# Performance work log

Measured on AMD Instinct MI355X. Metric: run time of the kernel, lower is better.

The kernel has to match this reference:

```python
import jax, jax.numpy as jnp
import numpy as np

K = 3
STRIDE = 1
PAD = 1
DIL = 1


def setup_inputs() -> dict:
    key = jax.random.key(0)
    k1, k2, k3 = jax.random.split(key, 3)
    B, C, O, H, W = 8, 64, 64, 128, 128
    x = jax.random.normal(k1, (B, C, H, W), dtype=jnp.float32)
    # small offset-conv weights so predicted offsets stay in a sane range
    w_off = jax.random.normal(k2, (2 * K * K, C, K, K), dtype=jnp.float32) * 0.05
    b_off = jnp.zeros((2 * K * K,), dtype=jnp.float32)
    w_conv = jax.random.normal(k3, (O, C, K, K), dtype=jnp.float32) * (1.0 / np.sqrt(C * K * K))
    return {"x": x, "w_off": w_off, "b_off": b_off, "w_conv": w_conv}


def _offset_conv(x, w, b):
    y = jax.lax.conv_general_dilated(
        x, w, window_strides=(STRIDE, STRIDE),
        padding=[(PAD, PAD), (PAD, PAD)], rhs_dilation=(DIL, DIL),
        dimension_numbers=("NCHW", "OIHW", "NCHW"))
    return y + b[None, :, None, None]


def _deform_conv2d(x, offset, weight):
    # torchvision deform_conv2d v1, groups=1, offset_groups=1, no bias
    B, C, H, W = x.shape
    Ho, Wo = offset.shape[2], offset.shape[3]
    # offset channels laid out as (ky, kx, [dy, dx]) pairs
    off = offset.reshape(B, K, K, 2, Ho, Wo)
    dy, dx = off[:, :, :, 0], off[:, :, :, 1]           # [B,K,K,Ho,Wo]

    hs = (jnp.arange(Ho) * STRIDE - PAD).astype(offset.dtype)
    ws = (jnp.arange(Wo) * STRIDE - PAD).astype(offset.dtype)
    kk = (jnp.arange(K) * DIL).astype(offset.dtype)
    py = hs[None, None, None, :, None] + kk[None, :, None, None, None] + dy
    px = ws[None, None, None, None, :] + kk[None, None, :, None, None] + dx

    y0 = jnp.floor(py)
    x0 = jnp.floor(px)
    ly = py - y0
    lx = px - x0
    y0i = y0.astype(jnp.int32)
    x0i = x0.astype(jnp.int32)

    xf = x.reshape(B, C, H * W)

    def gather(yi, xi):
        valid = ((yi >= 0) & (yi < H) & (xi >= 0) & (xi < W)).astype(x.dtype)
        idx = jnp.clip(yi, 0, H - 1) * W + jnp.clip(xi, 0, W - 1)  # [B,K,K,Ho,Wo]
        idxf = idx.reshape(B, 1, -1)
        v = jnp.take_along_axis(xf, idxf, axis=2)                  # [B,C,K*K*Ho*Wo]
        v = v.reshape(B, C, K, K, Ho, Wo)
        return v * valid[:, None]                                  # zero-pad out of bounds

    ly_ = ly[:, None]  # broadcast over channel dim
    lx_ = lx[:, None]
    val = (gather(y0i, x0i) * (1 - ly_) * (1 - lx_)
           + gather(y0i, x0i + 1) * (1 - ly_) * lx_
           + gather(y0i + 1, x0i) * ly_ * (1 - lx_)
           + gather(y0i + 1, x0i + 1) * ly_ * lx_)   # [B,C,K,K,Ho,Wo]

    return jnp.einsum("bcklhw,ockl->bohw", val, weight)


def reference(x, w_off, b_off, w_conv):
    offset = _offset_conv(x, w_off, b_off)
    return _deform_conv2d(x, offset, w_conv)
```

## Files before the change

### kernel.cpp

```cpp
#include <hip/hip_runtime.h>

#define B_    8
#define C_    64
#define O_    64
#define H_    128
#define W_    128
#define HW_   (H_ * W_)
#define NOFF_ 18
#define KK_   9
#define TW_   19
#define PADW_ 5
#define RSTR_ 144

typedef __attribute__((ext_vector_type(8))) _Float16 f16x8;
typedef __attribute__((ext_vector_type(2))) _Float16 f16x2;
typedef __attribute__((ext_vector_type(4))) unsigned int u32x4;
typedef __attribute__((ext_vector_type(4))) float f32x4;
typedef unsigned int uint32;
typedef unsigned short ushort;

__device__ __forceinline__ f16x2 u2h(uint32 u) {
    union { uint32 u; f16x2 h; } c; c.u = u; return c.h;
}
__device__ __forceinline__ f16x8 u2h8(u32x4 q) {
    union { u32x4 u; f16x8 h; } c; c.u = q; return c.h;
}

#define GLOAD16(dst, a64) \
    asm volatile("global_load_dwordx4 %0, %1, off" : "=&v"(dst) : "v"(a64) : "memory")
#define WAITV_TIE(N, w) \
    asm volatile("s_waitcnt vmcnt(" #N ")" \
        : "+v"(w[0]), "+v"(w[1]), "+v"(w[2]), "+v"(w[3]), \
          "+v"(w[4]), "+v"(w[5]), "+v"(w[6]), "+v"(w[7]))
#define WAITV(N) do { \
    asm volatile("s_waitcnt vmcnt(" #N ")" ::: "memory"); \
    __builtin_amdgcn_sched_barrier(0); } while (0)
#define DRAIN_ALL() do { \
    asm volatile("s_waitcnt vmcnt(0) lgkmcnt(0)" ::: "memory"); \
    __builtin_amdgcn_sched_barrier(0); } while (0)

__global__ __launch_bounds__(256) void transpose_x(
    const float* __restrict__ x, _Float16* __restrict__ xT)
{
    __shared__ float tile[64][65];
    int blk = blockIdx.x;
    int b   = blk >> 8;
    int hw0 = (blk & 255) * 64;
    int t   = threadIdx.x;
    int q   = t >> 6;
    int ln  = t & 63;
#pragma unroll
    for (int p = 0; p < 16; ++p) {
        int c = p * 4 + q;
        tile[c][ln] = x[((size_t)(b * C_ + c) << 14) + hw0 + ln];
    }
    __syncthreads();
#pragma unroll
    for (int p = 0; p < 16; ++p) {
        int hw = p * 4 + q;
        xT[(((size_t)b << 14) + hw0 + hw) * 64 + ln] = (_Float16)tile[ln][hw];
    }
}

__global__ __launch_bounds__(256) void prep3(
    const float* __restrict__ w_conv, const float* __restrict__ w_off,
    _Float16* __restrict__ wfrag, _Float16* __restrict__ wofff)
{
    int idx = blockIdx.x * 256 + threadIdx.x;
    if (idx < 36864) {
        int i    = idx & 7;
        int lane = (idx >> 3) & 63;
        int nb   = (idx >> 9) & 3;
        int kc   = (idx >> 11) & 1;
        int kk   = idx >> 12;
        int c = kc * 32 + ((lane >> 4) << 3) + i;
        int o = nb * 16 + (lane & 15);
        wfrag[idx] = (_Float16)w_conv[(o * C_ + c) * 9 + kk];
    }
    if (idx < 18432) {
        int i    = idx & 7;
        int lane = (idx >> 3) & 63;
        int nb   = (idx >> 9) & 1;
        int kc   = (idx >> 10) & 1;
        int kk   = idx >> 11;
        int m = nb * 16 + (lane & 15);
        int c = kc * 32 + ((lane >> 4) << 3) + i;
        wofff[idx] = (_Float16)((m < NOFF_) ? w_off[(m * C_ + c) * 9 + kk] : 0.0f);
    }
}

__global__ __launch_bounds__(512, 2) void offconv_mfma5(
    const _Float16* __restrict__ xT, const _Float16* __restrict__ wofff,
    const float* __restrict__ b_off, _Float16* __restrict__ offsh)
{
    __shared__ _Float16 wlds[18432];
    int t = threadIdx.x;
    {
        const u32x4* src = (const u32x4*)wofff;
        u32x4* dst = (u32x4*)wlds;
#pragma unroll
        for (int r = 0; r < 5; ++r) {
            int i = r * 512 + t;
            if (i < 2304) dst[i] = src[i];
        }
    }
    DRAIN_ALL();
    __syncthreads();

    int blk  = blockIdx.x;
    int b    = blk & 7;
    int hw0  = (blk >> 3) * 128;
    int lane = t & 63;
    int wv   = t >> 6;
    int pxb  = hw0 + wv * 16;
    int pr   = lane & 15;
    int g    = lane >> 4;
    int px   = pxb + pr;
    int h = px >> 7, w = px & (W_ - 1);
    const _Float16* xb = xT + (((size_t)b << 14) << 6);

    f32x4 acc[2];
#pragma unroll
    for (int nb = 0; nb < 2; ++nb) acc[nb] = (f32x4){0.f, 0.f, 0.f, 0.f};

    u32x4 q[3][2];
    bool  vld[3];

    auto issueO = [&](int kk, int st) {
        int ky = kk / 3, kx = kk % 3;
        int yy = h - 1 + ky, xx = w - 1 + kx;
        vld[st] = ((unsigned)yy < (unsigned)H_) && ((unsigned)xx < (unsigned)W_);
        int src = (min(max(yy, 0), H_ - 1) << 7) + min(max(xx, 0), W_ - 1);
        unsigned long long a = (unsigned long long)(xb + ((size_t)src << 6) + g * 8);
        GLOAD16(q[st][0], a);
        unsigned long long a2 = a + 64;
        GLOAD16(q[st][1], a2);
    };

    issueO(0, 0); issueO(1, 1); issueO(2, 2);
#pragma unroll
    for (int kk = 0; kk < KK_; ++kk) {
        const int s = kk % 3;
        if (kk < 7)      { WAITV(4); }
        else if (kk < 8) { WAITV(2); }
        else             { WAITV(0); }
#pragma unroll
        for (int kc = 0; kc < 2; ++kc) {
            f16x8 a = u2h8(q[s][kc]);
            f16x8 z = {};
            a = vld[s] ? a : z;
#pragma unroll
            for (int nb = 0; nb < 2; ++nb) {
                f16x8 bfr = *(const f16x8*)(wlds +
                    ((((kk * 2 + kc) << 1) + nb) << 9) + (lane << 3));
                acc[nb] = __builtin_amdgcn_mfma_f32_16x16x32_f16(a, bfr, acc[nb], 0, 0, 0);
            }
        }
        if (kk < 6) issueO(kk + 3, s);
    }

#pragma unroll
    for (int nb = 0; nb < 2; ++nb) {
        int m = nb * 16 + pr;
        if (m < NOFF_) {
            float bias = b_off[m];
#pragma unroll
            for (int r = 0; r < 4; ++r) {
                int prow = pxb + g * 4 + r;
                offsh[(size_t)((b << 14) + prow) * NOFF_ + m] = (_Float16)(acc[nb][r] + bias);
            }
        }
    }
}

__global__ __launch_bounds__(256, 2) void deform_mfma12(
    const _Float16* __restrict__ xT, const _Float16* __restrict__ offsh,
    const _Float16* __restrict__ wfrag, float* __restrict__ out)
{
    __shared__ char tilec[TW_ * TW_ * RSTR_];

    int t    = threadIdx.x;
    int blk  = blockIdx.x;
    int b    = blk & 7;
    int tid  = blk >> 3;
    int ty   = tid >> 4, tx = tid & 15;
    int lane = t & 63;
    int wv   = t >> 6;
    int pr   = lane & 15;
    int gg   = lane >> 4;
    int ry0  = ty * 8 - PADW_;
    int cx0  = tx * 8 - PADW_;
    const _Float16* xb = xT + (((size_t)b << 14) << 6);

#pragma unroll
    for (int it = 0; it < 12; ++it) {
        int idx = it * 256 + t;
        if (idx < TW_ * TW_ * 8) {
            int i   = idx / (TW_ * 8);
            int rem = idx - i * (TW_ * 8);
            int j   = rem >> 3, cg = rem & 7;
            int yy = min(max(ry0 + i, 0), H_ - 1);
            int xx = min(max(cx0 + j, 0), W_ - 1);
            u32x4 v = *(const u32x4*)(xb + (((size_t)((yy << 7) + xx)) << 6) + (cg << 3));
            int rl = i * TW_ + j;
            *(u32x4*)(tilec + rl * RSTR_ + (cg << 4)) = v;
        }
    }

    int h_img = ty * 8 + wv * 2 + (pr >> 3);
    int w_img = tx * 8 + (pr & 7);
    const uint32* obu = (const uint32*)(offsh +
        (size_t)((b << 14) + (h_img << 7) + w_img) * NOFF_);
    uint32 dpk[9];
#pragma unroll
    for (int kk = 0; kk < 9; ++kk) dpk[kk] = obu[kk];
    DRAIN_ALL();
    __syncthreads();

    f32x4 acc[4];
#pragma unroll
    for (int nb = 0; nb < 4; ++nb) acc[nb] = (f32x4){0.f, 0.f, 0.f, 0.f};

    auto prepk = [&](int kk, f16x2* Wc, int* rlc, int* ycx) -> int {
        int ky = kk / 3, kx = kk % 3;
        union { uint32 u; f16x2 hh; } cv; cv.u = dpk[kk];
        float dyv = (float)cv.hh[0], dxv = (float)cv.hh[1];
        float py  = (float)(h_img - 1 + ky) + dyv;
        float pxf = (float)(w_img - 1 + kx) + dxv;
        float y0f = floorf(py), x0f = floorf(pxf);
        float ly = py - y0f, lx = pxf - x0f;
        int y0 = (int)y0f, x0 = (int)x0f;
        float w00 = (1.f - ly) * (1.f - lx);
        float w01 = (1.f - ly) * lx;
        float w10 = ly * (1.f - lx);
        float w11 = ly * lx;
        bool vy0 = (unsigned)y0       < (unsigned)H_;
        bool vy1 = (unsigned)(y0 + 1) < (unsigned)H_;
        bool vx0 = (unsigned)x0       < (unsigned)W_;
        bool vx1 = (unsigned)(x0 + 1) < (unsigned)W_;
        if (!(vy0 && vx0)) w00 = 0.f;
        if (!(vy0 && vx1)) w01 = 0.f;
        if (!(vy1 && vx0)) w10 = 0.f;
        if (!(vy1 && vx1)) w11 = 0.f;
        int yc0 = min(max(y0, 0), H_ - 1);
        int yc1 = min(max(y0 + 1, 0), H_ - 1);
        int xc0 = min(max(x0, 0), W_ - 1);
        int xc1 = min(max(x0 + 1, 0), W_ - 1);
        Wc[0] = (f16x2){(_Float16)w00, (_Float16)w00};
        Wc[1] = (f16x2){(_Float16)w01, (_Float16)w01};
        Wc[2] = (f16x2){(_Float16)w10, (_Float16)w10};
        Wc[3] = (f16x2){(_Float16)w11, (_Float16)w11};
        ycx[0] = yc0; ycx[1] = yc1; ycx[2] = xc0; ycx[3] = xc1;
        int r0 = yc0 - ry0, r1 = yc1 - ry0;
        int c0 = xc0 - cx0, c1 = xc1 - cx0;
        int bad = ((unsigned)r0 >= TW_) | ((unsigned)r1 >= TW_) |
                  ((unsigned)c0 >= TW_) | ((unsigned)c1 >= TW_);
        r0 = min(max(r0, 0), TW_ - 1); r1 = min(max(r1, 0), TW_ - 1);
        c0 = min(max(c0, 0), TW_ - 1); c1 = min(max(c1, 0), TW_ - 1);
        rlc[0] = r0 * TW_ + c0; rlc[1] = r0 * TW_ + c1;
        rlc[2] = r1 * TW_ + c0; rlc[3] = r1 * TW_ + c1;
        return bad;
    };
    auto ldsRead = [&](const int* rlc, u32x4* q) {
#pragma unroll
        for (int kc = 0; kc < 2; ++kc) {
            int ch = (gg << 4) + (kc << 6);
#pragma unroll
            for (int cr = 0; cr < 4; ++cr)
                q[kc * 4 + cr] = *(const u32x4*)(tilec + rlc[cr] * RSTR_ + ch);
        }
    };
    auto issueW = [&](int kk, u32x4* wq) {
#pragma unroll
        for (int f = 0; f < 8; ++f) {
            unsigned long long wa = (unsigned long long)(wfrag +
                ((((kk * 2 + (f >> 2)) << 2) + (f & 3)) << 9) + (lane << 3));
            GLOAD16(wq[f], wa);
        }
    };
    auto bilerp = [&](const u32x4* q, const f16x2* Wc, int kc) -> f16x8 {
        f16x8 a;
        f16x2* ap = (f16x2*)&a;
#pragma unroll
        for (int p4 = 0; p4 < 4; ++p4) {
            ap[p4] = u2h(q[kc * 4 + 0][p4]) * Wc[0]
                   + u2h(q[kc * 4 + 1][p4]) * Wc[1]
                   + u2h(q[kc * 4 + 2][p4]) * Wc[2]
                   + u2h(q[kc * 4 + 3][p4]) * Wc[3];
        }
        return a;
    };

    u32x4 qA[8], qB[8], wqA[8], wqB[8];
    f16x2 WcA[4], WcB[4];
    int   rlA[4], rlB[4], ycxT[4];
    uint32 badmask = 0;

    issueW(0, wqA);
    if (prepk(0, WcA, rlA, ycxT)) badmask |= 1u;
    ldsRead(rlA, qA);

#pragma unroll
    for (int kk = 0; kk < KK_; ++kk) {
        u32x4* wcur = (kk & 1) ? wqB : wqA;
        u32x4* wnxt = (kk & 1) ? wqA : wqB;
        u32x4* qcur = (kk & 1) ? qB : qA;
        u32x4* qnxt = (kk & 1) ? qA : qB;
        f16x2* Wcur = (kk & 1) ? WcB : WcA;
        f16x2* Wnxt = (kk & 1) ? WcA : WcB;
        int*   rlnx = (kk & 1) ? rlA : rlB;

        if (kk < 8) {
            issueW(kk + 1, wnxt);
            if (prepk(kk + 1, Wnxt, rlnx, ycxT)) badmask |= (1u << (kk + 1));
            ldsRead(rlnx, qnxt);
        }

        f16x8 a0 = bilerp(qcur, Wcur, 0);
        f16x8 a1 = bilerp(qcur, Wcur, 1);

        if (kk < 8) { WAITV_TIE(8, wcur); } else { WAITV_TIE(0, wcur); }

#pragma unroll
        for (int nb = 0; nb < 4; ++nb)
            acc[nb] = __builtin_amdgcn_mfma_f32_16x16x32_f16(a0, u2h8(wcur[nb]), acc[nb], 0, 0, 0);
#pragma unroll
        for (int nb = 0; nb < 4; ++nb)
            acc[nb] = __builtin_amdgcn_mfma_f32_16x16x32_f16(a1, u2h8(wcur[4 + nb]), acc[nb], 0, 0, 0);
    }

    if (__any((int)(badmask != 0))) {
#pragma unroll 1
        for (int kk = 0; kk < KK_; ++kk) {
            int mybad = (badmask >> kk) & 1;
            if (__any(mybad)) {
                f16x2 Wc[4]; int rlc[4], ycx[4];
                prepk(kk, Wc, rlc, ycx);
                u32x4 qw[8], qr[8];
                ldsRead(rlc, qw);
#pragma unroll
                for (int kc = 0; kc < 2; ++kc) {
                    int ce = ((kc << 2) + gg) << 3;
#pragma unroll
                    for (int cr = 0; cr < 4; ++cr) {
                        int yy = ycx[cr >> 1], xx = ycx[2 + (cr & 1)];
                        unsigned long long a = (unsigned long long)(xb +
                            (((size_t)((yy << 7) + xx)) << 6) + ce);
                        GLOAD16(qr[kc * 4 + cr], a);
                    }
                }
                issueW(kk, wqA);
                WAITV(0);
#pragma unroll
                for (int kc = 0; kc < 2; ++kc) {
                    f16x8 aw = bilerp(qw, Wc, kc);
                    f16x8 ar = bilerp(qr, Wc, kc);
                    f16x8 d  = ar - aw;
                    f16x8 z  = {};
                    d = mybad ? d : z;
#pragma unroll
                    for (int nb = 0; nb < 4; ++nb)
                        acc[nb] = __builtin_amdgcn_mfma_f32_16x16x32_f16(
                            d, u2h8(wqA[kc * 4 + nb]), acc[nb], 0, 0, 0);
                }
            }
        }
    }

#pragma unroll
    for (int nb = 0; nb < 4; ++nb) {
        int o = nb * 16 + pr;
        int orow = ty * 8 + wv * 2 + (gg >> 1);
        int ocol = tx * 8 + ((gg & 1) << 2);
        float* outp = out + (((size_t)(b * O_ + o)) << 14) + (orow << 7) + ocol;
        *(f32x4*)outp = acc[nb];
    }
}

extern "C" void kernel_launch(void* const* d_in, const int* in_sizes, int n_in,
                              void* d_out, int out_size, void* d_ws, size_t ws_size,
                              hipStream_t stream)
{
    const float* x      = (const float*)d_in[0];
    const float* w_off  = (const float*)d_in[1];
    const float* b_off  = (const float*)d_in[2];
    const float* w_conv = (const float*)d_in[3];
    float* out = (float*)d_out;
    char* ws = (char*)d_ws;

    const size_t XT_OFF    = 0;
    const size_t OFFS_OFF  = 16777216;
    const size_t WFRAG_OFF = 21495808;
    const size_t WOFF_OFF  = 21569536;

    _Float16* xT    = (_Float16*)(ws + XT_OFF);
    _Float16* offsh = (_Float16*)(ws + OFFS_OFF);
    _Float16* wfrag = (_Float16*)(ws + WFRAG_OFF);
    _Float16* wofff = (_Float16*)(ws + WOFF_OFF);

    transpose_x  <<<2048, 256, 0, stream>>>(x, xT);
    prep3        <<<144, 256, 0, stream>>>(w_conv, w_off, wfrag, wofff);
    offconv_mfma5<<<1024, 512, 0, stream>>>(xT, wofff, b_off, offsh);
    deform_mfma12<<<2048, 256, 0, stream>>>(xT, offsh, wfrag, out);
}
```

Baseline: 68.67 us.

## Split kernel taps across three wave groups with LDS reduction in deform conv

The deform kernel now runs 768 threads per block: each of the four pixel-row waves is replicated three times, and each replica handles three of the nine kernel taps (one ky row). Partial MFMA accumulators from the second and third groups are reduced through LDS, reusing the tile buffer, and the first group writes the output. The aim is more parallelism per block and shorter per-wave serial MFMA chains, which should hide latency better. The cost is extra syncthreads, an LDS reduction pass, and higher register pressure under launch_bounds(768,3), which may reduce occupancy.

```diff
diff --git a/kernel.cpp b/kernel.cpp
--- a/kernel.cpp
+++ b/kernel.cpp
@@ -173,7 +173,7 @@
     }
 }
 
-__global__ __launch_bounds__(256, 2) void deform_mfma12(
+__global__ __launch_bounds__(768, 3) void deform_mfma13(
     const _Float16* __restrict__ xT, const _Float16* __restrict__ offsh,
     const _Float16* __restrict__ wfrag, float* __restrict__ out)
 {
@@ -186,6 +186,8 @@
     int ty   = tid >> 4, tx = tid & 15;
     int lane = t & 63;
     int wv   = t >> 6;
+    int pxg  = wv & 3;
+    int kkg  = wv >> 2;
     int pr   = lane & 15;
     int gg   = lane >> 4;
     int ry0  = ty * 8 - PADW_;
@@ -193,8 +195,8 @@
     const _Float16* xb = xT + (((size_t)b << 14) << 6);
 
 #pragma unroll
-    for (int it = 0; it < 12; ++it) {
-        int idx = it * 256 + t;
+    for (int it = 0; it < 4; ++it) {
+        int idx = it * 768 + t;
         if (idx < TW_ * TW_ * 8) {
             int i   = idx / (TW_ * 8);
             int rem = idx - i * (TW_ * 8);
@@ -207,13 +209,14 @@
         }
     }
 
-    int h_img = ty * 8 + wv * 2 + (pr >> 3);
+    int h_img = ty * 8 + pxg * 2 + (pr >> 3);
     int w_img = tx * 8 + (pr & 7);
     const uint32* obu = (const uint32*)(offsh +
         (size_t)((b << 14) + (h_img << 7) + w_img) * NOFF_);
-    uint32 dpk[9];
-#pragma unroll
-    for (int kk = 0; kk < 9; ++kk) dpk[kk] = obu[kk];
+    const int k0 = kkg * 3;
+    uint32 dpk[3];
+#pragma unroll
+    for (int i = 0; i < 3; ++i) dpk[i] = obu[k0 + i];
     DRAIN_ALL();
     __syncthreads();
 
@@ -221,9 +224,10 @@
 #pragma unroll
     for (int nb = 0; nb < 4; ++nb) acc[nb] = (f32x4){0.f, 0.f, 0.f, 0.f};
 
-    auto prepk = [&](int kk, f16x2* Wc, int* rlc, int* ycx) -> int {
+    auto prepk = [&](int ki, f16x2* Wc, int* rlc, int* ycx) -> int {
+        int kk = k0 + ki;
         int ky = kk / 3, kx = kk % 3;
-        union { uint32 u; f16x2 hh; } cv; cv.u = dpk[kk];
+        union { uint32 u; f16x2 hh; } cv; cv.u = dpk[ki];
         float dyv = (float)cv.hh[0], dxv = (float)cv.hh[1];
         float py  = (float)(h_img - 1 + ky) + dyv;
         float pxf = (float)(w_img - 1 + kx) + dxv;
@@ -296,30 +300,30 @@
     int   rlA[4], rlB[4], ycxT[4];
     uint32 badmask = 0;
 
-    issueW(0, wqA);
+    issueW(k0, wqA);
     if (prepk(0, WcA, rlA, ycxT)) badmask |= 1u;
     ldsRead(rlA, qA);
 
 #pragma unroll
-    for (int kk = 0; kk < KK_; ++kk) {
-        u32x4* wcur = (kk & 1) ? wqB : wqA;
-        u32x4* wnxt = (kk & 1) ? wqA : wqB;
-        u32x4* qcur = (kk & 1) ? qB : qA;
-        u32x4* qnxt = (kk & 1) ? qA : qB;
-        f16x2* Wcur = (kk & 1) ? WcB : WcA;
-        f16x2* Wnxt = (kk & 1) ? WcA : WcB;
-        int*   rlnx = (kk & 1) ? rlA : rlB;
-
-        if (kk < 8) {
-            issueW(kk + 1, wnxt);
-            if (prepk(kk + 1, Wnxt, rlnx, ycxT)) badmask |= (1u << (kk + 1));
+    for (int ki = 0; ki < 3; ++ki) {
+        u32x4* wcur = (ki & 1) ? wqB : wqA;
+        u32x4* wnxt = (ki & 1) ? wqA : wqB;
+        u32x4* qcur = (ki & 1) ? qB : qA;
+        u32x4* qnxt = (ki & 1) ? qA : qB;
+        f16x2* Wcur = (ki & 1) ? WcB : WcA;
+        f16x2* Wnxt = (ki & 1) ? WcA : WcB;
+        int*   rlnx = (ki & 1) ? rlA : rlB;
+
+        if (ki < 2) {
+            issueW(k0 + ki + 1, wnxt);
+            if (prepk(ki + 1, Wnxt, rlnx, ycxT)) badmask |= (1u << (ki + 1));
             ldsRead(rlnx, qnxt);
         }
 
         f16x8 a0 = bilerp(qcur, Wcur, 0);
         f16x8 a1 = bilerp(qcur, Wcur, 1);
 
-        if (kk < 8) { WAITV_TIE(8, wcur); } else { WAITV_TIE(0, wcur); }
+        if (ki < 2) { WAITV_TIE(8, wcur); } else { WAITV_TIE(0, wcur); }
 
 #pragma unroll
         for (int nb = 0; nb < 4; ++nb)
@@ -331,11 +335,11 @@
 
     if (__any((int)(badmask != 0))) {
 #pragma unroll 1
-        for (int kk = 0; kk < KK_; ++kk) {
-            int mybad = (badmask >> kk) & 1;
+        for (int ki = 0; ki < 3; ++ki) {
+            int mybad = (badmask >> ki) & 1;
             if (__any(mybad)) {
                 f16x2 Wc[4]; int rlc[4], ycx[4];
-                prepk(kk, Wc, rlc, ycx);
+                prepk(ki, Wc, rlc, ycx);
                 u32x4 qw[8], qr[8];
                 ldsRead(rlc, qw);
 #pragma unroll
@@ -349,7 +353,7 @@
                         GLOAD16(qr[kc * 4 + cr], a);
                     }
                 }
-                issueW(kk, wqA);
+                issueW(k0 + ki, wqA);
                 WAITV(0);
 #pragma unroll
                 for (int kc = 0; kc < 2; ++kc) {
@@ -367,13 +371,31 @@
         }
     }
 
-#pragma unroll
-    for (int nb = 0; nb < 4; ++nb) {
-        int o = nb * 16 + pr;
-        int orow = ty * 8 + wv * 2 + (gg >> 1);
-        int ocol = tx * 8 + ((gg & 1) << 2);
-        float* outp = out + (((size_t)(b * O_ + o)) << 14) + (orow << 7) + ocol;
-        *(f32x4*)outp = acc[nb];
+    __syncthreads();
+    if (kkg > 0) {
+        char* sl = tilec + ((pxg * 2 + (kkg - 1)) << 12);
+#pragma unroll
+        for (int nb = 0; nb < 4; ++nb)
+            *(f32x4*)(sl + nb * 1024 + (lane << 4)) = acc[nb];
+    }
+    __syncthreads();
+    if (kkg == 0) {
+        char* s0 = tilec + ((pxg * 2 + 0) << 12);
+        char* s1 = tilec + ((pxg * 2 + 1) << 12);
+#pragma unroll
+        for (int nb = 0; nb < 4; ++nb) {
+            f32x4 v0 = *(const f32x4*)(s0 + nb * 1024 + (lane << 4));
+            f32x4 v1 = *(const f32x4*)(s1 + nb * 1024 + (lane << 4));
+            acc[nb] += v0 + v1;
+        }
+#pragma unroll
+        for (int nb = 0; nb < 4; ++nb) {
+            int o = nb * 16 + pr;
+            int orow = ty * 8 + pxg * 2 + (gg >> 1);
+            int ocol = tx * 8 + ((gg & 1) << 2);
+            float* outp = out + (((size_t)(b * O_ + o)) << 14) + (orow << 7) + ocol;
+            *(f32x4*)outp = acc[nb];
+        }
     }
 }
 
@@ -401,5 +423,5 @@
     transpose_x  <<<2048, 256, 0, stream>>>(x, xT);
     prep3        <<<144, 256, 0, stream>>>(w_conv, w_off, wfrag, wofff);
     offconv_mfma5<<<1024, 512, 0, stream>>>(xT, wofff, b_off, offsh);
-    deform_mfma12<<<2048, 256, 0, stream>>>(xT, offsh, wfrag, out);
-}
+    deform_mfma13<<<2048, 768, 0, stream>>>(xT, offsh, wfrag, out);
+}
```

Measured after the change: 77.58 us. 13.0% more time.

## Fuse offset convolution into deform kernel using the shared-memory input tile

Applied to the files above, without the earlier changes.

Removes the separate offset-conv kernel and its fp16 offset buffer. The deform kernel now computes each tile's 18 offset channels with MFMA, reading input from the halo tile it already stages in LDS. Offset weights are streamed from global memory with double buffering, and results go through a small LDS array kept in fp32. This saves a launch and the offset write and read round trip, at the cost of extra per-block MFMA work and a higher occupancy target of 3 blocks per SM.

```diff
diff --git a/kernel.cpp b/kernel.cpp
--- a/kernel.cpp
+++ b/kernel.cpp
@@ -32,8 +32,14 @@
     asm volatile("s_waitcnt vmcnt(" #N ")" \
         : "+v"(w[0]), "+v"(w[1]), "+v"(w[2]), "+v"(w[3]), \
           "+v"(w[4]), "+v"(w[5]), "+v"(w[6]), "+v"(w[7]))
+#define WAITV_TIE4(N, w) \
+    asm volatile("s_waitcnt vmcnt(" #N ")" \
+        : "+v"(w[0]), "+v"(w[1]), "+v"(w[2]), "+v"(w[3]))
 #define WAITV(N) do { \
     asm volatile("s_waitcnt vmcnt(" #N ")" ::: "memory"); \
+    __builtin_amdgcn_sched_barrier(0); } while (0)
+#define WAITLGKM0() do { \
+    asm volatile("s_waitcnt lgkmcnt(0)" ::: "memory"); \
     __builtin_amdgcn_sched_barrier(0); } while (0)
 #define DRAIN_ALL() do { \
     asm volatile("s_waitcnt vmcnt(0) lgkmcnt(0)" ::: "memory"); \
@@ -89,95 +95,13 @@
     }
 }
 
-__global__ __launch_bounds__(512, 2) void offconv_mfma5(
-    const _Float16* __restrict__ xT, const _Float16* __restrict__ wofff,
-    const float* __restrict__ b_off, _Float16* __restrict__ offsh)
+__global__ __launch_bounds__(256, 3) void deform_fused(
+    const _Float16* __restrict__ xT, const _Float16* __restrict__ wfrag,
+    const _Float16* __restrict__ wofff, const float* __restrict__ b_off,
+    float* __restrict__ out)
 {
-    __shared__ _Float16 wlds[18432];
-    int t = threadIdx.x;
-    {
-        const u32x4* src = (const u32x4*)wofff;
-        u32x4* dst = (u32x4*)wlds;
-#pragma unroll
-        for (int r = 0; r < 5; ++r) {
-            int i = r * 512 + t;
-            if (i < 2304) dst[i] = src[i];
-        }
-    }
-    DRAIN_ALL();
-    __syncthreads();
-
-    int blk  = blockIdx.x;
-    int b    = blk & 7;
-    int hw0  = (blk >> 3) * 128;
-    int lane = t & 63;
-    int wv   = t >> 6;
-    int pxb  = hw0 + wv * 16;
-    int pr   = lane & 15;
-    int g    = lane >> 4;
-    int px   = pxb + pr;
-    int h = px >> 7, w = px & (W_ - 1);
-    const _Float16* xb = xT + (((size_t)b << 14) << 6);
-
-    f32x4 acc[2];
-#pragma unroll
-    for (int nb = 0; nb < 2; ++nb) acc[nb] = (f32x4){0.f, 0.f, 0.f, 0.f};
-
-    u32x4 q[3][2];
-    bool  vld[3];
-
-    auto issueO = [&](int kk, int st) {
-        int ky = kk / 3, kx = kk % 3;
-        int yy = h - 1 + ky, xx = w - 1 + kx;
-        vld[st] = ((unsigned)yy < (unsigned)H_) && ((unsigned)xx < (unsigned)W_);
-        int src = (min(max(yy, 0), H_ - 1) << 7) + min(max(xx, 0), W_ - 1);
-        unsigned long long a = (unsigned long long)(xb + ((size_t)src << 6) + g * 8);
-        GLOAD16(q[st][0], a);
-        unsigned long long a2 = a + 64;
-        GLOAD16(q[st][1], a2);
-    };
-
-    issueO(0, 0); issueO(1, 1); issueO(2, 2);
-#pragma unroll
-    for (int kk = 0; kk < KK_; ++kk) {
-        const int s = kk % 3;
-        if (kk < 7)      { WAITV(4); }
-        else if (kk < 8) { WAITV(2); }
-        else             { WAITV(0); }
-#pragma unroll
-        for (int kc = 0; kc < 2; ++kc) {
-            f16x8 a = u2h8(q[s][kc]);
-            f16x8 z = {};
-            a = vld[s] ? a : z;
-#pragma unroll
-            for (int nb = 0; nb < 2; ++nb) {
-                f16x8 bfr = *(const f16x8*)(wlds +
-                    ((((kk * 2 + kc) << 1) + nb) << 9) + (lane << 3));
-                acc[nb] = __builtin_amdgcn_mfma_f32_16x16x32_f16(a, bfr, acc[nb], 0, 0, 0);
-            }
-        }
-        if (kk < 6) issueO(kk + 3, s);
-    }
-
-#pragma unroll
-    for (int nb = 0; nb < 2; ++nb) {
-        int m = nb * 16 + pr;
-        if (m < NOFF_) {
-            float bias = b_off[m];
-#pragma unroll
-            for (int r = 0; r < 4; ++r) {
-                int prow = pxb + g * 4 + r;
-                offsh[(size_t)((b << 14) + prow) * NOFF_ + m] = (_Float16)(acc[nb][r] + bias);
-            }
-        }
-    }
-}
-
-__global__ __launch_bounds__(256, 2) void deform_mfma12(
-    const _Float16* __restrict__ xT, const _Float16* __restrict__ offsh,
-    const _Float16* __restrict__ wfrag, float* __restrict__ out)
-{
-    __shared__ char tilec[TW_ * TW_ * RSTR_];
+    __shared__ char  tilec[TW_ * TW_ * RSTR_];
+    __shared__ float offl[4][16][20];
 
     int t    = threadIdx.x;
     int blk  = blockIdx.x;
@@ -192,6 +116,9 @@
     int cx0  = tx * 8 - PADW_;
     const _Float16* xb = xT + (((size_t)b << 14) << 6);
 
+    float bias0 = b_off[pr];
+    float bias1 = (pr < 2) ? b_off[16 + pr] : 0.0f;
+
 #pragma unroll
     for (int it = 0; it < 12; ++it) {
         int idx = it * 256 + t;
@@ -209,24 +136,74 @@
 
     int h_img = ty * 8 + wv * 2 + (pr >> 3);
     int w_img = tx * 8 + (pr & 7);
-    const uint32* obu = (const uint32*)(offsh +
-        (size_t)((b << 14) + (h_img << 7) + w_img) * NOFF_);
-    uint32 dpk[9];
-#pragma unroll
-    for (int kk = 0; kk < 9; ++kk) dpk[kk] = obu[kk];
     DRAIN_ALL();
     __syncthreads();
 
+    {
+        f32x4 acco[2];
+        acco[0] = (f32x4){0.f, 0.f, 0.f, 0.f};
+        acco[1] = (f32x4){0.f, 0.f, 0.f, 0.f};
+
+        u32x4 wqoA[4], wqoB[4];
+        auto issueWO = [&](int kk, u32x4* wq) {
+#pragma unroll
+            for (int f = 0; f < 4; ++f) {
+                unsigned long long wa = (unsigned long long)(wofff +
+                    ((((kk * 2 + (f >> 1)) << 1) + (f & 1)) << 9) + (lane << 3));
+                GLOAD16(wq[f], wa);
+            }
+        };
+
+        issueWO(0, wqoA);
+#pragma unroll
+        for (int kk = 0; kk < KK_; ++kk) {
+            u32x4* wcur = (kk & 1) ? wqoB : wqoA;
+            u32x4* wnxt = (kk & 1) ? wqoA : wqoB;
+            if (kk < 8) issueWO(kk + 1, wnxt);
+
+            int ky = kk / 3, kx = kk % 3;
+            int yy = h_img - 1 + ky, xx = w_img - 1 + kx;
+            bool valid = ((unsigned)yy < (unsigned)H_) && ((unsigned)xx < (unsigned)W_);
+            int rl = (yy - ry0) * TW_ + (xx - cx0);
+            u32x4 q0 = *(const u32x4*)(tilec + rl * RSTR_ + (gg << 4));
+            u32x4 q1 = *(const u32x4*)(tilec + rl * RSTR_ + 64 + (gg << 4));
+            f16x8 a0 = u2h8(q0), a1 = u2h8(q1);
+            f16x8 z = {};
+            a0 = valid ? a0 : z;
+            a1 = valid ? a1 : z;
+
+            if (kk < 8) { WAITV_TIE4(4, wcur); } else { WAITV_TIE4(0, wcur); }
+
+            acco[0] = __builtin_amdgcn_mfma_f32_16x16x32_f16(a0, u2h8(wcur[0]), acco[0], 0, 0, 0);
+            acco[1] = __builtin_amdgcn_mfma_f32_16x16x32_f16(a0, u2h8(wcur[1]), acco[1], 0, 0, 0);
+            acco[0] = __builtin_amdgcn_mfma_f32_16x16x32_f16(a1, u2h8(wcur[2]), acco[0], 0, 0, 0);
+            acco[1] = __builtin_amdgcn_mfma_f32_16x16x32_f16(a1, u2h8(wcur[3]), acco[1], 0, 0, 0);
+        }
+
+#pragma unroll
+        for (int r = 0; r < 4; ++r) {
+            int pxl = gg * 4 + r;
+            offl[wv][pxl][pr] = acco[0][r] + bias0;
+            if (pr < 2) offl[wv][pxl][16 + pr] = acco[1][r] + bias1;
+        }
+        WAITLGKM0();
+    }
+
+    float dy[9], dx[9];
+#pragma unroll
+    for (int kk = 0; kk < 9; ++kk) {
+        float2 dd = *(const float2*)&offl[wv][pr][2 * kk];
+        dy[kk] = dd.x; dx[kk] = dd.y;
+    }
+
     f32x4 acc[4];
 #pragma unroll
     for (int nb = 0; nb < 4; ++nb) acc[nb] = (f32x4){0.f, 0.f, 0.f, 0.f};
 
     auto prepk = [&](int kk, f16x2* Wc, int* rlc, int* ycx) -> int {
         int ky = kk / 3, kx = kk % 3;
-        union { uint32 u; f16x2 hh; } cv; cv.u = dpk[kk];
-        float dyv = (float)cv.hh[0], dxv = (float)cv.hh[1];
-        float py  = (float)(h_img - 1 + ky) + dyv;
-        float pxf = (float)(w_img - 1 + kx) + dxv;
+        float py  = (float)(h_img - 1 + ky) + dy[kk];
+        float pxf = (float)(w_img - 1 + kx) + dx[kk];
         float y0f = floorf(py), x0f = floorf(pxf);
         float ly = py - y0f, lx = pxf - x0f;
         int y0 = (int)y0f, x0 = (int)x0f;
@@ -389,17 +366,14 @@
     char* ws = (char*)d_ws;
 
     const size_t XT_OFF    = 0;
-    const size_t OFFS_OFF  = 16777216;
     const size_t WFRAG_OFF = 21495808;
     const size_t WOFF_OFF  = 21569536;
 
     _Float16* xT    = (_Float16*)(ws + XT_OFF);
-    _Float16* offsh = (_Float16*)(ws + OFFS_OFF);
     _Float16* wfrag = (_Float16*)(ws + WFRAG_OFF);
     _Float16* wofff = (_Float16*)(ws + WOFF_OFF);
 
-    transpose_x  <<<2048, 256, 0, stream>>>(x, xT);
-    prep3        <<<144, 256, 0, stream>>>(w_conv, w_off, wfrag, wofff);
-    offconv_mfma5<<<1024, 512, 0, stream>>>(xT, wofff, b_off, offsh);
-    deform_mfma12<<<2048, 256, 0, stream>>>(xT, offsh, wfrag, out);
-}
+    transpose_x <<<2048, 256, 0, stream>>>(x, xT);
+    prep3       <<<144, 256, 0, stream>>>(w_conv, w_off, wfrag, wofff);
+    deform_fused<<<2048, 256, 0, stream>>>(xT, wfrag, wofff, b_off, out);
+}
```

After: 72.00 us. 1.05x slower.
